# Optimization experiments

Measured on AMD Instinct MI355X. Metric: run time of the kernel, lower is better.

## Reference

```python
import jax, jax.numpy as jnp
import numpy as np

B, S, NUM_TYPES, NUM_NODES, FREQ = 8, 2048, 8, 32, 256
COMP_R, COMP_L, COMP_C = 0, 1, 2
LS = 0.1  # label smoothing
W_TYPE, W_NODE, W_VAL, W_IMP, W_D1, W_D2, W_SELF, W_DUP = 1.0, 1.0, 0.5, 1.0, 0.5, 0.3, 2.0, 1.0


def setup_inputs() -> dict:
    key = jax.random.key(0)
    ks = jax.random.split(key, 9)
    type_logits = jax.random.normal(ks[0], (B, S, NUM_TYPES), jnp.float32)
    node_a_logits = jax.random.normal(ks[1], (B, S, NUM_NODES), jnp.float32)
    node_b_logits = jax.random.normal(ks[2], (B, S, NUM_NODES), jnp.float32)
    values = jax.random.normal(ks[3], (B, S, 1), jnp.float32)
    t_type = jax.random.randint(ks[4], (B, S, 1), 0, NUM_TYPES)
    t_na = jax.random.randint(ks[5], (B, S, 1), 0, NUM_NODES)
    t_nb = jax.random.randint(ks[6], (B, S, 1), 0, NUM_NODES)
    t_val = jax.random.normal(ks[7], (B, S, 1), jnp.float32)
    target_seq = jnp.concatenate(
        [t_type.astype(jnp.float32), t_na.astype(jnp.float32), t_nb.astype(jnp.float32), t_val], axis=-1)
    ki = jax.random.split(ks[8], 2)
    pred_impedance = jax.random.normal(ki[0], (B, 2, FREQ), jnp.float32)
    target_impedance = jax.random.normal(ki[1], (B, 2, FREQ), jnp.float32)
    return {"type_logits": type_logits, "node_a_logits": node_a_logits,
            "node_b_logits": node_b_logits, "values": values, "target_seq": target_seq,
            "pred_impedance": pred_impedance, "target_impedance": target_impedance}


def _ce_smooth(logits, targets):
    # torch CrossEntropyLoss(label_smoothing=LS), mean reduction
    logp = jax.nn.log_softmax(logits, axis=-1)
    nll = -jnp.take_along_axis(logp, targets[..., None], axis=-1)[..., 0]
    smooth = -jnp.mean(logp, axis=-1)
    return jnp.mean((1.0 - LS) * nll + LS * smooth)


def _mse(a, b):
    return jnp.mean((a - b) ** 2)


def _losses(type_logits, node_a_logits, node_b_logits, values,
            pred_impedance, target_impedance, target_seq):
    target_types = target_seq[:, :, 0].astype(jnp.int32)
    target_na = target_seq[:, :, 1].astype(jnp.int32)
    target_nb = target_seq[:, :, 2].astype(jnp.int32)
    target_values = target_seq[:, :, 3:4]

    type_loss = _ce_smooth(type_logits, target_types)
    node_a_loss = _ce_smooth(node_a_logits, target_na)
    node_b_loss = _ce_smooth(node_b_logits, target_nb)
    value_loss = _mse(values, target_values)

    # validity penalties
    pa = jax.nn.softmax(node_a_logits, axis=-1)  # [B,S,N]
    pb = jax.nn.softmax(node_b_logits, axis=-1)
    pt = jax.nn.softmax(type_logits, axis=-1)
    comp_mask = pt[:, :, COMP_R] + pt[:, :, COMP_L] + pt[:, :, COMP_C]  # [B,S]

    selfloop_prob = jnp.sum(pa * pb, axis=-1)  # [B,S]
    selfloop_penalty = jnp.mean(selfloop_prob * comp_mask)

    # edge_probs[b,s] = outer(pa,pb) + outer(pa,pb).T, flattened to [B,S,N*N]
    outer = jnp.einsum('bsi,bsj->bsij', pa, pb)
    edge = (outer + jnp.swapaxes(outer, -1, -2)).reshape(B, S, NUM_NODES * NUM_NODES)
    em = edge * comp_mask[..., None]  # fold comp weight into edge vectors
    gram = jnp.einsum('bsk,btk->bst', em, em)  # [B,S,S]
    trace = jnp.einsum('bss->b', gram)
    pair_sum = 0.5 * (jnp.sum(gram) - jnp.sum(trace))
    duplicate_penalty = pair_sum / (B * S * (S - 1) / 2 + 1e-8)

    # impedance derivative losses
    pm, tm = pred_impedance[:, 0, :], target_impedance[:, 0, :]
    pp, tp = pred_impedance[:, 1, :], target_impedance[:, 1, :]
    mag_loss = _mse(pm, tm)
    pd1, td1 = pm[:, 1:] - pm[:, :-1], tm[:, 1:] - tm[:, :-1]
    d1_loss = _mse(pd1, td1)
    d2_loss = _mse(pd1[:, 1:] - pd1[:, :-1], td1[:, 1:] - td1[:, :-1])
    phase_loss = _mse(pp, tp)

    total = (W_TYPE * type_loss + W_NODE * (node_a_loss + node_b_loss)
             + W_VAL * value_loss + W_SELF * selfloop_penalty
             + W_DUP * duplicate_penalty + W_IMP * mag_loss
             + W_D1 * d1_loss + W_D2 * d2_loss + 0.1 * phase_loss)
    return (total, type_loss, node_a_loss, node_b_loss, value_loss,
            selfloop_penalty, duplicate_penalty, mag_loss, d1_loss, d2_loss, phase_loss)


def reference(type_logits, node_a_logits, node_b_logits, values, target_seq,
              pred_impedance, target_impedance):
    return _losses(type_logits, node_a_logits, node_b_logits, values,
                   pred_impedance, target_impedance, target_seq)
```

## Files before the change

### kernel.cpp

```cpp
#include <hip/hip_runtime.h>


#define BB 8
#define SS 2048
#define NT 8
#define NN 32
#define FQ 256
#define NPOS (BB*SS)
#define NSLOT 256
#define WS_USLOT 0
#define WS_SSLOT (NSLOT*1024)
#define WS_BATCH (WS_SSLOT + NSLOT*8)
#define WS_TICKET (WS_BATCH + BB*16)

constexpr float LS_ = 0.1f;

__device__ __forceinline__ float softmax32(const float* __restrict__ src, int pos,
                                           int tgt, float* __restrict__ p) {
    const float4* q = reinterpret_cast<const float4*>(src) + pos * 8;
    #pragma unroll
    for (int i = 0; i < 8; i++) {
        float4 v = q[i];
        p[4*i] = v.x; p[4*i+1] = v.y; p[4*i+2] = v.z; p[4*i+3] = v.w;
    }
    float mx = p[0], sx = 0.f, pt = 0.f;
    #pragma unroll
    for (int i = 0; i < NN; i++) { mx = fmaxf(mx, p[i]); sx += p[i]; }
    #pragma unroll
    for (int i = 0; i < NN; i++) { pt = (i == tgt) ? p[i] : pt; }
    float es = 0.f;
    #pragma unroll
    for (int i = 0; i < NN; i++) { float e = __expf(p[i] - mx); p[i] = e; es += e; }
    const float inv = 1.f / es;
    #pragma unroll
    for (int i = 0; i < NN; i++) p[i] *= inv;
    const float logZ = mx + __logf(es);
    return (1.f - LS_) * (logZ - pt) + LS_ * (logZ - sx * (1.f / NN));
}

__global__ __launch_bounds__(64) void ck_main(
    const float* __restrict__ type_logits,
    const float* __restrict__ na_logits,
    const float* __restrict__ nb_logits,
    const float* __restrict__ values,
    const float* __restrict__ target_seq,
    float* __restrict__ ws)
{
    const int tid = threadIdx.x;
    const int bid = blockIdx.x;
    const int b   = bid >> 5;
    const int s   = ((bid & 31) << 6) + tid;
    const int pos = b * SS + s;

    if (tid == 0 && bid == 0) {
        *reinterpret_cast<int*>(ws + WS_TICKET) = 0;
    }

    const float4 tg = reinterpret_cast<const float4*>(target_seq)[pos];
    const float vv = values[pos];
    const int tt = (int)tg.x;
    const int ta = (int)tg.y;
    const int tb = (int)tg.z;
    const float tv = tg.w;

    float x[NT];
    {
        const float4* p = reinterpret_cast<const float4*>(type_logits) + pos * 2;
        float4 v0 = p[0], v1 = p[1];
        x[0]=v0.x; x[1]=v0.y; x[2]=v0.z; x[3]=v0.w;
        x[4]=v1.x; x[5]=v1.y; x[6]=v1.z; x[7]=v1.w;
    }
    float xmax = x[0], xs = 0.f, xt = 0.f;
    #pragma unroll
    for (int i = 0; i < NT; i++) { xmax = fmaxf(xmax, x[i]); xs += x[i]; }
    #pragma unroll
    for (int i = 0; i < NT; i++) { xt = (i == tt) ? x[i] : xt; }
    float es = 0.f, e012 = 0.f;
    #pragma unroll
    for (int i = 0; i < NT; i++) {
        float e = __expf(x[i] - xmax);
        es += e;
        if (i < 3) e012 += e;
    }
    const float logZt = xmax + __logf(es);
    const float lt = (1.f - LS_) * (logZt - xt) + LS_ * (logZt - xs * (1.f / NT));
    const float m = e012 / es;

    float pa[NN], pb[NN];
    const float la = softmax32(na_logits, pos, ta, pa);
    const float lb = softmax32(nb_logits, pos, tb, pb);

    float Sa = 0.f, Sb = 0.f, dot = 0.f;
    #pragma unroll
    for (int i = 0; i < NN; i++) {
        Sa = fmaf(pa[i], pa[i], Sa);
        Sb = fmaf(pb[i], pb[i], Sb);
        dot = fmaf(pa[i], pb[i], dot);
    }
    const float self = m * dot;
    const float tr   = 2.f * m * m * (Sa * Sb + dot * dot);
    const float dv   = vv - tv;
    const float vsq  = dv * dv;

    float r0 = lt, r1 = la, r2 = lb, r3 = vsq, r4 = self, r5 = tr;
    #pragma unroll
    for (int o = 32; o > 0; o >>= 1) {
        r0 += __shfl_down(r0, o); r1 += __shfl_down(r1, o);
        r2 += __shfl_down(r2, o); r3 += __shfl_down(r3, o);
        r4 += __shfl_down(r4, o); r5 += __shfl_down(r5, o);
    }
    if (tid == 0) {
        float* sp = ws + WS_SSLOT + bid * 8;
        sp[0]=r0; sp[1]=r1; sp[2]=r2; sp[3]=r3; sp[4]=r4; sp[5]=r5;
    }

    __shared__ float4 lpa[64][9];
    __shared__ float4 lpb[64][9];
    #pragma unroll
    for (int q = 0; q < 8; q++) {
        lpa[tid][q] = make_float4(m*pa[4*q], m*pa[4*q+1], m*pa[4*q+2], m*pa[4*q+3]);
        lpb[tid][q] = make_float4(pb[4*q], pb[4*q+1], pb[4*q+2], pb[4*q+3]);
    }
    __syncthreads();

    const int i4 = tid >> 3;
    const int j4 = tid & 7;
    float acc[4][4];
    #pragma unroll
    for (int ii = 0; ii < 4; ii++)
        #pragma unroll
        for (int jj = 0; jj < 4; jj++) acc[ii][jj] = 0.f;
    for (int t = 0; t < 64; t++) {
        float4 av = lpa[t][i4];
        float4 bv = lpb[t][j4];
        const float aa[4] = {av.x, av.y, av.z, av.w};
        const float bbv[4] = {bv.x, bv.y, bv.z, bv.w};
        #pragma unroll
        for (int ii = 0; ii < 4; ii++)
            #pragma unroll
            for (int jj = 0; jj < 4; jj++)
                acc[ii][jj] = fmaf(aa[ii], bbv[jj], acc[ii][jj]);
    }
    float4* slot = reinterpret_cast<float4*>(ws + WS_USLOT + bid * 1024);
    #pragma unroll
    for (int ii = 0; ii < 4; ii++)
        slot[((i4*4+ii)*32 + j4*4) >> 2] =
            make_float4(acc[ii][0], acc[ii][1], acc[ii][2], acc[ii][3]);
}

__device__ __forceinline__ float blk_reduce256(float v, float* lds) {
    #pragma unroll
    for (int o = 32; o > 0; o >>= 1) v += __shfl_down(v, o);
    const int tid = threadIdx.x;
    __syncthreads();
    if ((tid & 63) == 0) lds[tid >> 6] = v;
    __syncthreads();
    return lds[0] + lds[1] + lds[2] + lds[3];
}

__global__ __launch_bounds__(256) void ck_batch(
    const float* __restrict__ pred_imp,
    const float* __restrict__ targ_imp,
    float* __restrict__ ws,
    float* __restrict__ out)
{
    const int tid = threadIdx.x;
    const int b   = blockIdx.x;
    __shared__ __align__(16) float Ub[1024];
    __shared__ float red[4];

    const float4* base4 = reinterpret_cast<const float4*>(
        ws + WS_USLOT + (size_t)b * 32 * 1024);
    float4 acc = make_float4(0.f, 0.f, 0.f, 0.f);
    #pragma unroll 4
    for (int sl = 0; sl < 32; sl++) {
        float4 v = base4[sl * 256 + tid];
        acc.x += v.x; acc.y += v.y; acc.z += v.z; acc.w += v.w;
    }
    reinterpret_cast<float4*>(Ub)[tid] = acc;
    __syncthreads();

    float gr = 0.f;
    #pragma unroll
    for (int r = 0; r < 4; r++) {
        const int e = 4 * tid + r;
        const int i = e >> 5, j = e & 31;
        const float u  = Ub[e];
        const float ut = Ub[(j << 5) | i];
        gr = fmaf(u, u, gr);
        gr = fmaf(u, ut, gr);
    }

    const float* pm = pred_imp + b * 2 * FQ;
    const float* tm = targ_imp + b * 2 * FQ;
    const int f = tid;
    const float p0 = pm[f], t0 = tm[f];
    const float dm = p0 - t0;
    const float dp = pm[FQ + f] - tm[FQ + f];
    float mag = dm * dm;
    float phs = dp * dp;
    float d1 = 0.f, d2 = 0.f;
    if (f < FQ - 1) {
        const float p1 = pm[f + 1], t1 = tm[f + 1];
        const float a = (p1 - p0) - (t1 - t0);
        d1 = a * a;
        if (f < FQ - 2) {
            const float p2 = pm[f + 2], t2 = tm[f + 2];
            const float c = (p2 - 2.f*p1 + p0) - (t2 - 2.f*t1 + t0);
            d2 = c * c;
        }
    }

    float s0=0.f, s1=0.f, s2=0.f, s3=0.f, s4=0.f, s5=0.f;
    if (tid < 32) {
        const float* sp = ws + WS_SSLOT + (b * 32 + tid) * 8;
        s0 = sp[0]; s1 = sp[1]; s2 = sp[2]; s3 = sp[3]; s4 = sp[4]; s5 = sp[5];
    }

    const float GR  = blk_reduce256(gr,  red);
    const float MAG = blk_reduce256(mag, red);
    const float PHS = blk_reduce256(phs, red);
    const float D1  = blk_reduce256(d1,  red);
    const float D2  = blk_reduce256(d2,  red);
    const float S0  = blk_reduce256(s0,  red);
    const float S1  = blk_reduce256(s1,  red);
    const float S2  = blk_reduce256(s2,  red);
    const float S3  = blk_reduce256(s3,  red);
    const float S4  = blk_reduce256(s4,  red);
    const float S5  = blk_reduce256(s5,  red);

    if (tid == 0) {
        float* o = ws + WS_BATCH + b * 16;
        o[0]=GR; o[1]=MAG; o[2]=PHS; o[3]=D1; o[4]=D2;
        o[5]=S0; o[6]=S1; o[7]=S2; o[8]=S3; o[9]=S4; o[10]=S5;

        __threadfence();
        int* ticket = reinterpret_cast<int*>(ws + WS_TICKET);
        const int old = atomicAdd(ticket, 1);
        if (old == BB - 1) {
            __threadfence();
            float GRt=0,MAGt=0,PHSt=0,D1t=0,D2t=0,T0=0,T1=0,T2=0,T3=0,T4=0,T5=0;
            #pragma unroll
            for (int k = 0; k < BB; k++) {
                const float* p = ws + WS_BATCH + k * 16;
                GRt+=p[0]; MAGt+=p[1]; PHSt+=p[2]; D1t+=p[3]; D2t+=p[4];
                T0+=p[5]; T1+=p[6]; T2+=p[7]; T3+=p[8]; T4+=p[9]; T5+=p[10];
            }
            const float invN = 1.f / (float)NPOS;
            const float type_loss = T0 * invN;
            const float na_loss   = T1 * invN;
            const float nb_loss   = T2 * invN;
            const float val_loss  = T3 * invN;
            const float self_p    = T4 * invN;
            const float trace     = T5;
            const float sum_gram  = 2.f * GRt;
            const float pair_sum  = 0.5f * (sum_gram - trace);
            const float dup   = pair_sum / ((float)BB * SS * (SS - 1) * 0.5f + 1e-8f);
            const float mag_l = MAGt / (float)(BB * FQ);
            const float d1_l  = D1t  / (float)(BB * (FQ - 1));
            const float d2_l  = D2t  / (float)(BB * (FQ - 2));
            const float ph_l  = PHSt / (float)(BB * FQ);
            const float total = 1.0f * type_loss + 1.0f * (na_loss + nb_loss)
                              + 0.5f * val_loss + 2.0f * self_p + 1.0f * dup
                              + 1.0f * mag_l + 0.5f * d1_l + 0.3f * d2_l + 0.1f * ph_l;
            out[0]=total; out[1]=type_loss; out[2]=na_loss; out[3]=nb_loss;
            out[4]=val_loss; out[5]=self_p; out[6]=dup; out[7]=mag_l;
            out[8]=d1_l; out[9]=d2_l; out[10]=ph_l;
        }
    }
}

extern "C" void kernel_launch(void* const* d_in, const int* in_sizes, int n_in,
                              void* d_out, int out_size, void* d_ws, size_t ws_size,
                              hipStream_t stream)
{
    const float* type_logits = (const float*)d_in[0];
    const float* na_logits   = (const float*)d_in[1];
    const float* nb_logits   = (const float*)d_in[2];
    const float* values      = (const float*)d_in[3];
    const float* target_seq  = (const float*)d_in[4];
    const float* pred_imp    = (const float*)d_in[5];
    const float* targ_imp    = (const float*)d_in[6];
    float* out = (float*)d_out;
    float* ws  = (float*)d_ws;

    ck_main<<<NSLOT, 64, 0, stream>>>(type_logits, na_logits, nb_logits,
                                      values, target_seq, ws);
    ck_batch<<<BB, 256, 0, stream>>>(pred_imp, targ_imp, ws, out);
}
```

Measured before the change: 82.03 us.

## Use 256-thread blocks in main kernel and pre-reduce Gram tiles in LDS

The main kernel now runs 64 blocks of 256 threads instead of 256 blocks of 64, with each wave computing its own 32x32 outer-product tile. The four wave tiles are summed in shared memory before one slot per block goes to the workspace. This cuts the per-batch slot count from 32 to 8, so the batch kernel reads less data. In exchange it uses more LDS per block, adds a block-wide sync, and launches fewer blocks, which may leave much of the GPU idle.

Result: faster. 79.85 us, median of 2 (-2.7%).

```diff
diff --git a/kernel.cpp b/kernel.cpp
--- a/kernel.cpp
+++ b/kernel.cpp
@@ -7,10 +7,12 @@
 #define NN 32
 #define FQ 256
 #define NPOS (BB*SS)
-#define NSLOT 256
+#define NBLK1 64
+#define NSLOT 64
+#define NWSLOT 256
 #define WS_USLOT 0
 #define WS_SSLOT (NSLOT*1024)
-#define WS_BATCH (WS_SSLOT + NSLOT*8)
+#define WS_BATCH (WS_SSLOT + NWSLOT*8)
 #define WS_TICKET (WS_BATCH + BB*16)
 
 constexpr float LS_ = 0.1f;
@@ -38,7 +40,7 @@
     return (1.f - LS_) * (logZ - pt) + LS_ * (logZ - sx * (1.f / NN));
 }
 
-__global__ __launch_bounds__(64) void ck_main(
+__global__ __launch_bounds__(256) void ck_main(
     const float* __restrict__ type_logits,
     const float* __restrict__ na_logits,
     const float* __restrict__ nb_logits,
@@ -46,11 +48,14 @@
     const float* __restrict__ target_seq,
     float* __restrict__ ws)
 {
-    const int tid = threadIdx.x;
-    const int bid = blockIdx.x;
-    const int b   = bid >> 5;
-    const int s   = ((bid & 31) << 6) + tid;
-    const int pos = b * SS + s;
+    const int tid  = threadIdx.x;
+    const int bid  = blockIdx.x;
+    const int w    = tid >> 6;
+    const int lane = tid & 63;
+    const int b    = bid >> 3;
+    const int s    = ((bid & 7) << 8) + tid;
+    const int pos  = b * SS + s;
+    const int gw   = bid * 4 + w;
 
     if (tid == 0 && bid == 0) {
         *reinterpret_cast<int*>(ws + WS_TICKET) = 0;
@@ -109,30 +114,30 @@
         r2 += __shfl_down(r2, o); r3 += __shfl_down(r3, o);
         r4 += __shfl_down(r4, o); r5 += __shfl_down(r5, o);
     }
-    if (tid == 0) {
-        float* sp = ws + WS_SSLOT + bid * 8;
+    if (lane == 0) {
+        float* sp = ws + WS_SSLOT + gw * 8;
         sp[0]=r0; sp[1]=r1; sp[2]=r2; sp[3]=r3; sp[4]=r4; sp[5]=r5;
     }
 
-    __shared__ float4 lpa[64][9];
-    __shared__ float4 lpb[64][9];
+    __shared__ float4 lpa[4][64][9];
+    __shared__ float4 lpb[4][64][9];
     #pragma unroll
     for (int q = 0; q < 8; q++) {
-        lpa[tid][q] = make_float4(m*pa[4*q], m*pa[4*q+1], m*pa[4*q+2], m*pa[4*q+3]);
-        lpb[tid][q] = make_float4(pb[4*q], pb[4*q+1], pb[4*q+2], pb[4*q+3]);
-    }
-    __syncthreads();
-
-    const int i4 = tid >> 3;
-    const int j4 = tid & 7;
+        lpa[w][lane][q] = make_float4(m*pa[4*q], m*pa[4*q+1], m*pa[4*q+2], m*pa[4*q+3]);
+        lpb[w][lane][q] = make_float4(pb[4*q], pb[4*q+1], pb[4*q+2], pb[4*q+3]);
+    }
+    __syncthreads();
+
+    const int i4 = lane >> 3;
+    const int j4 = lane & 7;
     float acc[4][4];
     #pragma unroll
     for (int ii = 0; ii < 4; ii++)
         #pragma unroll
         for (int jj = 0; jj < 4; jj++) acc[ii][jj] = 0.f;
     for (int t = 0; t < 64; t++) {
-        float4 av = lpa[t][i4];
-        float4 bv = lpb[t][j4];
+        float4 av = lpa[w][t][i4];
+        float4 bv = lpb[w][t][j4];
         const float aa[4] = {av.x, av.y, av.z, av.w};
         const float bbv[4] = {bv.x, bv.y, bv.z, bv.w};
         #pragma unroll
@@ -141,11 +146,25 @@
             for (int jj = 0; jj < 4; jj++)
                 acc[ii][jj] = fmaf(aa[ii], bbv[jj], acc[ii][jj]);
     }
-    float4* slot = reinterpret_cast<float4*>(ws + WS_USLOT + bid * 1024);
+
+    __shared__ __align__(16) float Ured[4][1024];
     #pragma unroll
     for (int ii = 0; ii < 4; ii++)
-        slot[((i4*4+ii)*32 + j4*4) >> 2] =
-            make_float4(acc[ii][0], acc[ii][1], acc[ii][2], acc[ii][3]);
+        #pragma unroll
+        for (int jj = 0; jj < 4; jj++)
+            Ured[w][(i4*4+ii)*32 + (j4*4+jj)] = acc[ii][jj];
+    __syncthreads();
+
+    {
+        const float4* u0 = reinterpret_cast<const float4*>(Ured[0]);
+        const float4* u1 = reinterpret_cast<const float4*>(Ured[1]);
+        const float4* u2 = reinterpret_cast<const float4*>(Ured[2]);
+        const float4* u3 = reinterpret_cast<const float4*>(Ured[3]);
+        float4 a = u0[tid], c = u1[tid], d = u2[tid], e = u3[tid];
+        float4 sum = make_float4(a.x+c.x+d.x+e.x, a.y+c.y+d.y+e.y,
+                                 a.z+c.z+d.z+e.z, a.w+c.w+d.w+e.w);
+        reinterpret_cast<float4*>(ws + WS_USLOT + bid * 1024)[tid] = sum;
+    }
 }
 
 __device__ __forceinline__ float blk_reduce256(float v, float* lds) {
@@ -170,10 +189,10 @@
     __shared__ float red[4];
 
     const float4* base4 = reinterpret_cast<const float4*>(
-        ws + WS_USLOT + (size_t)b * 32 * 1024);
+        ws + WS_USLOT + (size_t)b * 8 * 1024);
     float4 acc = make_float4(0.f, 0.f, 0.f, 0.f);
-    #pragma unroll 4
-    for (int sl = 0; sl < 32; sl++) {
+    #pragma unroll
+    for (int sl = 0; sl < 8; sl++) {
         float4 v = base4[sl * 256 + tid];
         acc.x += v.x; acc.y += v.y; acc.z += v.z; acc.w += v.w;
     }
@@ -284,7 +303,7 @@
     float* out = (float*)d_out;
     float* ws  = (float*)d_ws;
 
-    ck_main<<<NSLOT, 64, 0, stream>>>(type_logits, na_logits, nb_logits,
-                                      values, target_seq, ws);
+    ck_main<<<NBLK1, 256, 0, stream>>>(type_logits, na_logits, nb_logits,
+                                       values, target_seq, ws);
     ck_batch<<<BB, 256, 0, stream>>>(pred_imp, targ_imp, ws, out);
 }
```
